# Kernel optimization log

Hardware: AMD Instinct MI355X
Metric: run time of the kernel (lower is better)

## Reference

```python
import jax, jax.numpy as jnp
from jax import lax
import numpy as np

DN = ('NCHW', 'OIHW', 'NCHW')
NUM_CLASSES = 80
TOPK = 100
EPS = 1e-6


def seek_local_maximum(x, eps=EPS):
    # x: [b, c, h, w]; 8-neighbor local-max with zero padding, like the torch code
    xp = jnp.pad(x, ((0, 0), (0, 0), (1, 1), (1, 1)))
    m = ((x >= xp[:, :, :-2, 1:-1]) & (x >= xp[:, :, 2:, 1:-1])
         & (x >= xp[:, :, 1:-1, :-2]) & (x >= xp[:, :, 1:-1, 2:])
         & (x >= xp[:, :, :-2, :-2]) & (x >= xp[:, :, :-2, 2:])
         & (x >= xp[:, :, 2:, :-2]) & (x >= xp[:, :, 2:, 2:])
         & (x >= eps))
    return m.astype(x.dtype)


def setup_inputs() -> dict:
    key = jax.random.key(0)
    k1, k2, k3, k4 = jax.random.split(key, 4)
    b, c, h, w = 8, 256, 100, 152
    nc1 = NUM_CLASSES + 1
    x = jax.random.normal(k1, (b, c, h, w), dtype=jnp.float32)
    pos_embeddings = jax.random.normal(k2, (1, c, h, w), dtype=jnp.float32)
    w1 = jax.random.normal(k3, (c, c, 3, 3), dtype=jnp.float32) * 0.02
    b1 = jnp.zeros((c,), dtype=jnp.float32)
    w2 = jax.random.normal(k4, (nc1, c, 1, 1), dtype=jnp.float32) * 0.02
    b2 = jnp.zeros((nc1,), dtype=jnp.float32)
    return {"x": x, "pos_embeddings": pos_embeddings, "w1": w1, "b1": b1, "w2": w2, "b2": b2}


def reference(x, pos_embeddings, w1, b1, w2, b2):
    b, c, h, w = x.shape
    # conv 3x3 + relu + conv 1x1 -> class logits [b, nc+1, h, w]
    hid = lax.conv_general_dilated(x, w1, (1, 1), 'SAME', dimension_numbers=DN)
    hid = jax.nn.relu(hid + b1[None, :, None, None])
    logits = lax.conv_general_dilated(hid, w2, (1, 1), 'SAME', dimension_numbers=DN)
    logits = logits + b2[None, :, None, None]
    probs = jax.nn.softmax(logits, axis=1)
    # one-hot of argmax over foreground classes (excluding last 'no-object' channel)
    cls_idx = jnp.argmax(probs[:, :-1], axis=1)                    # [b, h, w]
    one_hot = jax.nn.one_hot(cls_idx, NUM_CLASSES + 1, dtype=probs.dtype)  # [b, h, w, nc+1]
    probs = probs * jnp.transpose(one_hot, (0, 3, 1, 2))
    probs = probs + seek_local_maximum(probs)
    # per-pixel foreground score, topk over spatial positions
    scores = jnp.max(probs[:, :-1], axis=1).reshape(b, h * w)      # [b, h*w]
    _, topk_idx = lax.top_k(scores, TOPK)                          # [b, topk]
    idx = topk_idx[:, None, :]                                     # [b, 1, topk]
    topk_proposals = jnp.take_along_axis(x.reshape(b, c, h * w), idx, axis=2)
    pos = jnp.broadcast_to(pos_embeddings, (b, c, h, w)).reshape(b, c, h * w)
    topk_pos_embeddings = jnp.take_along_axis(pos, idx, axis=2)
    # eval mode: topk_locations is None in the torch module; omit it
    return (topk_proposals, topk_pos_embeddings, logits)
```

## Files before the change

### kernel.cpp

```cpp
#include <hip/hip_runtime.h>
#include <hip/hip_bf16.h>

#define Hh    100
#define Ww    152
#define Pp    15200
#define Cc    256
#define NBATCH 8
#define NC1   81
#define NCLS  80
#define KTOP  100

#define PROWS 102
#define PCOLS 154
#define PIXB  1024
#define XT_BATCH_BYTES ((size_t)PROWS * PCOLS * PIXB)

typedef __attribute__((ext_vector_type(8))) short  bf16x8;
typedef __attribute__((ext_vector_type(4))) float  f32x4;

__device__ __forceinline__ unsigned short bf16_bits(float v) {
    __hip_bfloat16 h = __float2bfloat16(v);
    return *(unsigned short*)&h;
}
__device__ __forceinline__ float bf16_back(float v) {
    __hip_bfloat16 h = __float2bfloat16(v);
    return __bfloat162float(h);
}

typedef __attribute__((address_space(1))) const void GV;
typedef __attribute__((address_space(3))) void LV;
__device__ __forceinline__ void gload_lds16(const void* g, void* l) {
    __builtin_amdgcn_global_load_lds((GV*)g, (LV*)l, 16, 0, 0);
}

__global__ void pack_w(const float* __restrict__ w1, unsigned short* __restrict__ wpk)
{
    int id = blockIdx.x * 256 + threadIdx.x;
    int k = id >> 8, c = id & 255;
#pragma unroll
    for (int t = 0; t < 9; ++t) {
        float v = w1[(size_t)(k * 256 + c) * 9 + t];
        unsigned short hi = bf16_bits(v);
        unsigned short lo = bf16_bits(v - bf16_back(v));
        int region = ((c >> 5) * 9 + t) * 2;
        int base   = region * 8192;
        int pos    = (k >> 4) * 512 + ((c >> 3) & 3) * 128 + (k & 15) * 8 + (c & 7);
        wpk[base + pos]        = hi;
        wpk[base + 8192 + pos] = lo;
    }
}

__global__ __launch_bounds__(256)
void pack_x(const float* __restrict__ x, unsigned short* __restrict__ xT)
{
    __shared__ float ls[64][257];
    const int tid   = threadIdx.x;
    const int chunk = blockIdx.x;
    const int row   = blockIdx.y;
    const int n     = blockIdx.z;
    const int c0    = chunk * 64;
    const int yy    = row - 1;
    const bool rowok = ((unsigned)yy < (unsigned)Hh);

    const int lanec = tid & 63;
    const int xx    = c0 + lanec - 1;
    const bool colok = ((unsigned)xx < (unsigned)Ww);
    const bool ok = rowok && colok;

    const size_t rbase = ((size_t)n * Cc) * Pp + (size_t)(rowok ? yy : 0) * Ww
                       + (size_t)(colok ? xx : 0);
#pragma unroll 4
    for (int i = 0; i < 64; ++i) {
        const int c = (tid >> 6) + i * 4;
        float v = 0.f;
        if (ok) v = x[rbase + (size_t)c * Pp];
        ls[lanec][c] = v;
    }
    __syncthreads();

    const int cch = tid;
#pragma unroll 1
    for (int j = 0; j < 64; ++j) {
        const int pc = c0 + j;
        if (pc >= PCOLS) break;
        float v = ls[j][cch];
        unsigned short hi = bf16_bits(v);
        unsigned short lo = bf16_bits(v - bf16_back(v));
        size_t dst = (((size_t)n * PROWS + row) * PCOLS + pc) * 512 + cch;
        xT[dst]       = hi;
        xT[dst + 256] = lo;
    }
}

#define BBUFB 49152

__global__ __launch_bounds__(512, 2)
void conv3x3_mfma(const unsigned short* __restrict__ xT,
                  const unsigned short* __restrict__ wpk,
                  const float* __restrict__ b1, float* __restrict__ hid)
{
    __shared__ f32x4 ldsbuf[6144];
    char* L = (char*)ldsbuf;

    const int tid  = threadIdx.x;
    const int lane = tid & 63;
    const int wv   = tid >> 6;
    const int wm   = wv >> 2;
    const int wn   = wv & 3;
    const int quad = lane >> 4, lq = lane & 15;

    const int bx = blockIdx.x;
    const int rb = bx / 5, cb = bx - rb * 5;
    const int y0 = rb * 8;
    const int x0 = cb * 32;
    const int k0 = blockIdx.y * 128;
    const int n  = blockIdx.z;

    const char* xb = (const char*)xT + (size_t)n * XT_BATCH_BYTES;
    const char* abase = (const char*)wpk + (size_t)(k0 >> 4) * 1024
                      + (size_t)(wm * 4) * 1024 + (size_t)lane * 16;

    const unsigned kslot = (lane & 7) ^ (lane >> 3);
    const size_t chnbase = (kslot < 4) ? (size_t)(kslot * 16)
                                       : (size_t)(448 + kslot * 16);

    auto stageB = [&](int s) {
        char* bdst = L + (size_t)(s & 1) * BBUFB;
        const size_t chn = (size_t)s * 64 + chnbase;
#pragma unroll
        for (int k6 = 0; k6 < 6; ++k6) {
            const int j   = wv + 8 * k6;
            const int pix = 8 * j + (lane >> 3);
            const int r   = pix / 34;
            const int c   = pix - r * 34;
            int prow = y0 + r; prow = prow < 102 ? prow : 101;
            const char* g = xb + (((size_t)(prow * 154 + x0 + c)) << 10) + chn;
            gload_lds16(g, bdst + (size_t)j * 1024);
        }
    };

    auto loadA = [&](int u, bf16x8 (&ah)[4], bf16x8 (&al)[4]) {
        const char* p0 = abase + (size_t)u * 32768;
#pragma unroll
        for (int m = 0; m < 4; ++m) {
            ah[m] = *(const bf16x8*)(p0 + m * 1024);
            al[m] = *(const bf16x8*)(p0 + m * 1024 + 16384);
        }
    };

    const int pix0 = wn * 2 * 34 + lq;
    auto readB = [&](int s, int t, bf16x8 (&bh)[4], bf16x8 (&bl)[4]) {
        const char* Bb = L + (size_t)(s & 1) * BBUFB;
        const int ty = t / 3, tx = t - ty * 3;
        const int pb0 = pix0 + ty * 34 + tx;
#pragma unroll
        for (int i = 0; i < 4; ++i) {
            const int pix = pb0 + (i >> 1) * 34 + (i & 1) * 16;
            const int a = pix * 128 + ((quad ^ (pix & 7)) << 4);
            bh[i] = *(const bf16x8*)(Bb + a);
            bl[i] = *(const bf16x8*)(Bb + (a ^ 64));
        }
    };

    f32x4 acc[4][4];
#pragma unroll
    for (int a = 0; a < 4; ++a)
#pragma unroll
        for (int b = 0; b < 4; ++b) acc[a][b] = 0;

    auto mfma48 = [&](bf16x8 (&ah)[4], bf16x8 (&al)[4],
                      bf16x8 (&bh)[4], bf16x8 (&bl)[4]) {
        __builtin_amdgcn_s_setprio(1);
#pragma unroll
        for (int m = 0; m < 4; ++m)
#pragma unroll
            for (int i = 0; i < 4; ++i)
                acc[m][i] = __builtin_amdgcn_mfma_f32_16x16x32_bf16(ah[m], bh[i], acc[m][i], 0, 0, 0);
#pragma unroll
        for (int m = 0; m < 4; ++m)
#pragma unroll
            for (int i = 0; i < 4; ++i)
                acc[m][i] = __builtin_amdgcn_mfma_f32_16x16x32_bf16(ah[m], bl[i], acc[m][i], 0, 0, 0);
#pragma unroll
        for (int m = 0; m < 4; ++m)
#pragma unroll
            for (int i = 0; i < 4; ++i)
                acc[m][i] = __builtin_amdgcn_mfma_f32_16x16x32_bf16(al[m], bh[i], acc[m][i], 0, 0, 0);
        __builtin_amdgcn_s_setprio(0);
    };

    bf16x8 ah[2][4], al[2][4], bh[2][4], bl[2][4];

    stageB(0);
    __syncthreads();
    loadA(0, ah[0], al[0]);
    readB(0, 0, bh[0], bl[0]);

#pragma unroll 1
    for (int s = 0; s < 8; ++s) {
        if (s < 7) stageB(s + 1);
#pragma unroll
        for (int t = 0; t < 9; ++t) {
            const int cur = t & 1, nx = cur ^ 1;
            if (t < 8) {
                loadA(s * 9 + t + 1, ah[nx], al[nx]);
                readB(s, t + 1, bh[nx], bl[nx]);
            }
            mfma48(ah[cur], al[cur], bh[cur], bl[cur]);
        }
        __syncthreads();
        if (s < 7) {
            loadA((s + 1) * 9, ah[0], al[0]);
            readB(s + 1, 0, bh[0], bl[0]);
        }
    }

#pragma unroll
    for (int m = 0; m < 4; ++m) {
        const int kb = k0 + wm * 64 + m * 16 + quad * 4;
        const float b0 = b1[kb], b1v = b1[kb + 1], b2v = b1[kb + 2], b3v = b1[kb + 3];
#pragma unroll
        for (int i = 0; i < 4; ++i) {
            const int y = y0 + wn * 2 + (i >> 1);
            const int xcol = x0 + (i & 1) * 16 + lq;
            if (y < Hh && xcol < Ww) {
                float* hp = hid + ((size_t)n * Cc + kb) * Pp + y * Ww + xcol;
                hp[0]              = fmaxf(acc[m][i].x + b0,  0.f);
                hp[Pp]             = fmaxf(acc[m][i].y + b1v, 0.f);
                hp[2 * Pp]         = fmaxf(acc[m][i].z + b2v, 0.f);
                hp[3 * (size_t)Pp] = fmaxf(acc[m][i].w + b3v, 0.f);
            }
        }
    }
}

__global__ __launch_bounds__(256, 2)
void conv1x1_softmax(const float* __restrict__ hid, const float* __restrict__ w2,
                     const float* __restrict__ b2, float* __restrict__ logits,
                     float* __restrict__ pmap, int* __restrict__ cmap)
{
    __shared__ float w2s[64 * 84];
    const int tid = threadIdx.x;
    const int p   = blockIdx.x * 256 + tid;
    const int n   = blockIdx.y;
    const bool valid = (p < Pp);
    const int psafe = valid ? p : 0;

    float acc[84];
#pragma unroll
    for (int j = 0; j < 84; ++j) acc[j] = 0.f;

#pragma unroll 1
    for (int c0 = 0; c0 < Cc; c0 += 64) {
        __syncthreads();
#pragma unroll
        for (int i = 0; i < 21; ++i) {
            int q  = i * 256 + tid;
            int cl = q / 84;
            int j  = q - cl * 84;
            float v = 0.f;
            if (j < NC1) v = w2[j * 256 + c0 + cl];
            w2s[cl * 84 + j] = v;
        }
        __syncthreads();

        const float* hptr = hid + ((size_t)n * Cc + c0) * Pp + psafe;
#pragma unroll 2
        for (int cl = 0; cl < 64; ++cl) {
            float h = hptr[(size_t)cl * Pp];
            const float4* wrow = (const float4*)(&w2s[cl * 84]);
#pragma unroll
            for (int f = 0; f < 21; ++f) {
                float4 wv = wrow[f];
                acc[f * 4 + 0] = fmaf(wv.x, h, acc[f * 4 + 0]);
                acc[f * 4 + 1] = fmaf(wv.y, h, acc[f * 4 + 1]);
                acc[f * 4 + 2] = fmaf(wv.z, h, acc[f * 4 + 2]);
                acc[f * 4 + 3] = fmaf(wv.w, h, acc[f * 4 + 3]);
            }
        }
    }

    if (valid) {
#pragma unroll
        for (int j = 0; j < NC1; ++j) acc[j] += b2[j];

        float* lp = logits + (size_t)n * NC1 * Pp + p;
#pragma unroll
        for (int j = 0; j < NC1; ++j) lp[(size_t)j * Pp] = acc[j];

        float m = -3.4e38f;
#pragma unroll
        for (int j = 0; j < NC1; ++j) m = fmaxf(m, acc[j]);
        float s = 0.f;
#pragma unroll
        for (int j = 0; j < NC1; ++j) s += __expf(acc[j] - m);
        float best = -3.4e38f; int bi = 0;
#pragma unroll
        for (int j = 0; j < NCLS; ++j) {
            if (acc[j] > best) { best = acc[j]; bi = j; }
        }
        pmap[n * Pp + p] = __expf(best - m) / s;
        cmap[n * Pp + p] = bi;
    }
}

__global__ void local_score(const float* __restrict__ pmap, const int* __restrict__ cmap,
                            float* __restrict__ scores)
{
    int p = blockIdx.x * 256 + threadIdx.x;
    int n = blockIdx.y;
    if (p >= Pp) return;
    int base = n * Pp;
    float pv = pmap[base + p];
    int   c  = cmap[base + p];
    int y = p / Ww, xc = p - y * Ww;
    bool ok = (pv >= 1e-6f);
#pragma unroll
    for (int dy = -1; dy <= 1; ++dy)
#pragma unroll
        for (int dx = -1; dx <= 1; ++dx) {
            if (dy == 0 && dx == 0) continue;
            int yy = y + dy, xx = xc + dx;
            if (yy >= 0 && yy < Hh && xx >= 0 && xx < Ww) {
                int q = base + yy * Ww + xx;
                if (cmap[q] == c && pmap[q] > pv) ok = false;
            }
        }
    scores[base + p] = pv + (ok ? 1.f : 0.f);
}

__global__ __launch_bounds__(256)
void topk_gather(const float* __restrict__ scores, const float* __restrict__ x,
                 const float* __restrict__ pos, float* __restrict__ oprop,
                 float* __restrict__ opos)
{
    __shared__ float sv[Pp];
    __shared__ int sidx[KTOP];
    __shared__ unsigned long long red[4];
    const int tid = threadIdx.x;
    const int n   = blockIdx.x;

    for (int i = tid; i < Pp; i += 256) sv[i] = scores[n * Pp + i];
    __syncthreads();

    for (int it = 0; it < KTOP; ++it) {
        unsigned long long best = 0ull;
        for (int i = tid; i < Pp; i += 256) {
            unsigned fb = __float_as_uint(sv[i]);
            unsigned long long key =
                ((unsigned long long)fb << 32) | (unsigned)(0xFFFF - i);
            best = key > best ? key : best;
        }
#pragma unroll
        for (int off = 32; off > 0; off >>= 1) {
            unsigned long long o = __shfl_down(best, off, 64);
            best = o > best ? o : best;
        }
        if ((tid & 63) == 0) red[tid >> 6] = best;
        __syncthreads();
        if (tid == 0) {
            unsigned long long b = red[0];
            b = red[1] > b ? red[1] : b;
            b = red[2] > b ? red[2] : b;
            b = red[3] > b ? red[3] : b;
            int idx = 0xFFFF - (int)(b & 0xFFFFFFFFull);
            sidx[it] = idx;
            sv[idx]  = 0.f;
        }
        __syncthreads();
    }

    for (int t = tid; t < Cc * KTOP; t += 256) {
        int c = t / KTOP;
        int i = t - c * KTOP;
        int idx = sidx[i];
        oprop[n * Cc * KTOP + c * KTOP + i] = x[((size_t)n * Cc + c) * Pp + idx];
        opos [n * Cc * KTOP + c * KTOP + i] = pos[(size_t)c * Pp + idx];
    }
}

extern "C" void kernel_launch(void* const* d_in, const int* in_sizes, int n_in,
                              void* d_out, int out_size, void* d_ws, size_t ws_size,
                              hipStream_t stream)
{
    const float* x   = (const float*)d_in[0];
    const float* pos = (const float*)d_in[1];
    const float* w1  = (const float*)d_in[2];
    const float* b1  = (const float*)d_in[3];
    const float* w2  = (const float*)d_in[4];
    const float* b2  = (const float*)d_in[5];

    float* out    = (float*)d_out;
    float* oprop  = out;
    float* oposE  = out + (size_t)NBATCH * Cc * KTOP;
    float* logits = out + (size_t)2 * NBATCH * Cc * KTOP;

    unsigned short* wpk = (unsigned short*)logits;

    float* ws  = (float*)d_ws;
    float* hid = ws;
    unsigned short* xT = (unsigned short*)(ws + (size_t)NBATCH * Cc * Pp);
    char* after_xt = (char*)xT + (size_t)NBATCH * XT_BATCH_BYTES;
    float* pmap   = (float*)after_xt;
    int*   cmap   = (int*)(pmap + (size_t)NBATCH * Pp);
    float* scores = (float*)(cmap + (size_t)NBATCH * Pp);

    pack_w<<<256, 256, 0, stream>>>(w1, wpk);
    pack_x<<<dim3(3, PROWS, NBATCH), 256, 0, stream>>>(x, xT);
    conv3x3_mfma<<<dim3(65, 2, NBATCH), 512, 0, stream>>>(
        xT, wpk, b1, hid);
    conv1x1_softmax<<<dim3((Pp + 255) / 256, NBATCH), 256, 0, stream>>>(
        hid, w2, b2, logits, pmap, cmap);
    local_score<<<dim3((Pp + 255) / 256, NBATCH), 256, 0, stream>>>(
        pmap, cmap, scores);
    topk_gather<<<NBATCH, 256, 0, stream>>>(scores, x, pos, oprop, oposE);
}
```

Before: 1.220 ms.

## Incremental top-k with cached per-thread maxima and XCD-aware conv block remap

The top-k kernel now uses 1024 threads and keeps each thread's running best key. After each selection, only the thread owning the chosen index rescans its slice, instead of every thread rescanning all scores per iteration. The conv grid is remapped so that consecutive hardware block ids spread across batches and channel halves, and sched_barriers pin the MFMA issue relative to the prefetch loads. The remap may change cache locality, and the sched barriers constrain compiler scheduling.

```diff
diff --git a/kernel.cpp b/kernel.cpp
--- a/kernel.cpp
+++ b/kernel.cpp
@@ -109,12 +109,17 @@
     const int wn   = wv & 3;
     const int quad = lane >> 4, lq = lane & 15;
 
-    const int bx = blockIdx.x;
+    const int hwflat  = blockIdx.x + 65 * (blockIdx.y + 2 * blockIdx.z);
+    const int logical = (hwflat & 7) * 130 + (hwflat >> 3);
+    const int n   = logical / 130;
+    const int rem = logical - n * 130;
+    const int bx  = rem >> 1;
+    const int k0b = rem & 1;
+
     const int rb = bx / 5, cb = bx - rb * 5;
     const int y0 = rb * 8;
     const int x0 = cb * 32;
-    const int k0 = blockIdx.y * 128;
-    const int n  = blockIdx.z;
+    const int k0 = k0b * 128;
 
     const char* xb = (const char*)xT + (size_t)n * XT_BATCH_BYTES;
     const char* abase = (const char*)wpk + (size_t)(k0 >> 4) * 1024
@@ -206,7 +211,9 @@
                 loadA(s * 9 + t + 1, ah[nx], al[nx]);
                 readB(s, t + 1, bh[nx], bl[nx]);
             }
+            __builtin_amdgcn_sched_barrier(0);
             mfma48(ah[cur], al[cur], bh[cur], bl[cur]);
+            __builtin_amdgcn_sched_barrier(0);
         }
         __syncthreads();
         if (s < 7) {
@@ -329,48 +336,63 @@
     scores[base + p] = pv + (ok ? 1.f : 0.f);
 }
 
-__global__ __launch_bounds__(256)
+__global__ __launch_bounds__(1024)
 void topk_gather(const float* __restrict__ scores, const float* __restrict__ x,
                  const float* __restrict__ pos, float* __restrict__ oprop,
                  float* __restrict__ opos)
 {
     __shared__ float sv[Pp];
     __shared__ int sidx[KTOP];
-    __shared__ unsigned long long red[4];
+    __shared__ unsigned long long red[16];
+    __shared__ unsigned long long bcast;
     const int tid = threadIdx.x;
     const int n   = blockIdx.x;
 
-    for (int i = tid; i < Pp; i += 256) sv[i] = scores[n * Pp + i];
+    for (int i = tid; i < Pp; i += 1024) sv[i] = scores[n * Pp + i];
     __syncthreads();
 
+    auto scan = [&]() -> unsigned long long {
+        unsigned long long best = 0ull;
+#pragma unroll
+        for (int k = 0; k < 15; ++k) {
+            const int i = tid + k * 1024;
+            if (i < Pp) {
+                unsigned fb = __float_as_uint(sv[i]);
+                unsigned long long key =
+                    ((unsigned long long)fb << 32) | (unsigned)(0xFFFF - i);
+                best = key > best ? key : best;
+            }
+        }
+        return best;
+    };
+
+    unsigned long long mybest = scan();
+
     for (int it = 0; it < KTOP; ++it) {
-        unsigned long long best = 0ull;
-        for (int i = tid; i < Pp; i += 256) {
-            unsigned fb = __float_as_uint(sv[i]);
-            unsigned long long key =
-                ((unsigned long long)fb << 32) | (unsigned)(0xFFFF - i);
-            best = key > best ? key : best;
-        }
+        unsigned long long b = mybest;
 #pragma unroll
         for (int off = 32; off > 0; off >>= 1) {
-            unsigned long long o = __shfl_down(best, off, 64);
-            best = o > best ? o : best;
-        }
-        if ((tid & 63) == 0) red[tid >> 6] = best;
+            unsigned long long o = __shfl_down(b, off, 64);
+            b = o > b ? o : b;
+        }
+        if ((tid & 63) == 0) red[tid >> 6] = b;
         __syncthreads();
         if (tid == 0) {
-            unsigned long long b = red[0];
-            b = red[1] > b ? red[1] : b;
-            b = red[2] > b ? red[2] : b;
-            b = red[3] > b ? red[3] : b;
-            int idx = 0xFFFF - (int)(b & 0xFFFFFFFFull);
+            unsigned long long bf = red[0];
+#pragma unroll
+            for (int w = 1; w < 16; ++w) bf = red[w] > bf ? red[w] : bf;
+            int idx = 0xFFFF - (int)(bf & 0xFFFFFFFFull);
             sidx[it] = idx;
             sv[idx]  = 0.f;
+            bcast    = bf;
         }
         __syncthreads();
-    }
-
-    for (int t = tid; t < Cc * KTOP; t += 256) {
+        const unsigned long long w = bcast;
+        const int idx = 0xFFFF - (int)(w & 0xFFFFFFFFull);
+        if ((idx & 1023) == tid) mybest = scan();
+    }
+
+    for (int t = tid; t < Cc * KTOP; t += 1024) {
         int c = t / KTOP;
         int i = t - c * KTOP;
         int idx = sidx[i];
@@ -413,5 +435,5 @@
         hid, w2, b2, logits, pmap, cmap);
     local_score<<<dim3((Pp + 255) / 256, NBATCH), 256, 0, stream>>>(
         pmap, cmap, scores);
-    topk_gather<<<NBATCH, 256, 0, stream>>>(scores, x, pos, oprop, oposE);
-}
+    topk_gather<<<NBATCH, 1024, 0, stream>>>(scores, x, pos, oprop, oposE);
+}
```

Result: faster. 1.136 ms (-6.8%).
